# Optimization experiments

Measured on AMD Instinct MI355X. Metric: run time of the kernel, lower is better.

The kernel has to match this reference:

```python
import jax, jax.numpy as jnp
import numpy as np

B, H, E, D = 16384, 1024, 64, 128  # batch, hidden, nb_entities, wh_units==we_units


def setup_inputs() -> dict:
    key = jax.random.key(0)
    k0, k1, k2 = jax.random.split(key, 3)
    hidden_state = jax.random.normal(k0, (B, H), dtype=jnp.float32)
    # Wh: Dense(wh_units) acting on H -> D
    Wh_w = jax.random.normal(k1, (H, D), dtype=jnp.float32) * 0.02
    Wh_b = jnp.zeros((D,), dtype=jnp.float32)
    # We: nb_entities separate Dense(we_units), stacked into one [E, D, D] tensor
    We_w = jax.random.normal(k2, (E, D, D), dtype=jnp.float32) * 0.02
    We_b = jnp.zeros((E, D), dtype=jnp.float32)
    return {"hidden_state": hidden_state, "Wh_w": Wh_w, "Wh_b": Wh_b,
            "We_w": We_w, "We_b": We_b}


def reference(hidden_state, Wh_w, Wh_b, We_w, We_b):
    # reduced_dimentionality = Wh(hidden_state)            [B, D]
    r = hidden_state @ Wh_w + Wh_b
    # per-entity Dense loop + concat + transpose == one batched GEMM -> [B, E, D]
    logits = jnp.einsum('bk,ekd->bed', r, We_w) + We_b[None, :, :]
    outputs = jax.nn.softmax(logits, axis=-1)               # [B, E, D]
    # second pass: We[i] applied to outputs[:, i, :]       [B, E, D]
    vt = jnp.einsum('bek,ekd->bed', outputs, We_w) + We_b[None, :, :]
    # transpose to [B, D, E] then reduce_sum over E == sum over entity axis
    result = vt.sum(axis=1)                                 # [B, D]
    return (outputs, result)
```

## Files before the change

### kernel.cpp

```cpp
#include <hip/hip_runtime.h>
#include <hip/hip_bf16.h>

typedef __attribute__((ext_vector_type(8))) short short8;
typedef __attribute__((ext_vector_type(4))) float f32x4;
typedef __attribute__((ext_vector_type(4))) unsigned int uint4v;
typedef __attribute__((ext_vector_type(2))) unsigned int uint2v;

#define NB 16384
#define NH 1024
#define NE 64
#define ND 128
#define BR 32

static __device__ __forceinline__ unsigned short f2b(float x) {
  unsigned int u = __builtin_bit_cast(unsigned int, x);
  unsigned int r = (u + 0x7fffu + ((u >> 16) & 1u)) >> 16;
  return (unsigned short)r;
}
static __device__ __forceinline__ float b2f_lo(unsigned int u) {
  return __builtin_bit_cast(float, u << 16);
}
static __device__ __forceinline__ float b2f_hi(unsigned int u) {
  return __builtin_bit_cast(float, u & 0xffff0000u);
}

static __device__ __forceinline__ void bar_sync() {
  __builtin_amdgcn_sched_barrier(0);
  asm volatile("s_waitcnt lgkmcnt(0)" ::: "memory");
  __builtin_amdgcn_sched_barrier(0);
  __builtin_amdgcn_s_barrier();
  __builtin_amdgcn_sched_barrier(0);
}

static __device__ __forceinline__ int swz(int row, int col) {
  return (row << 7) + ((((col >> 3) ^ (row & 7)) << 3) | (col & 7));
}

__global__ __launch_bounds__(256, 1) void k0_prep(
    const float* __restrict__ Wh_w, const float* __restrict__ We_w,
    const float* __restrict__ We_b,
    unsigned short* __restrict__ WeT, unsigned short* __restrict__ WhT,
    float* __restrict__ bsum)
{
  __shared__ float tile[32][33];
  const int bid = blockIdx.x, t = threadIdx.x;
  const int i = t >> 5, j = t & 31;
  if (bid < 1024) {
    const int e = bid >> 4, tr = (bid >> 2) & 3, tc = bid & 3;
    const float* src = We_w + (size_t)e * 16384;
#pragma unroll
    for (int k = 0; k < 4; ++k)
      tile[i + 8 * k][j] = src[(size_t)(tr * 32 + i + 8 * k) * 128 + tc * 32 + j];
    __syncthreads();
    unsigned short* dst = WeT + (size_t)e * 16384;
#pragma unroll
    for (int k = 0; k < 4; ++k) {
      int row = i + 8 * k;
      dst[(size_t)(tc * 32 + row) * 128 + tr * 32 + j] = f2b(tile[j][row]);
    }
  } else if (bid < 1152) {
    const int tb = bid - 1024, tr = tb >> 2, tc = tb & 3;
#pragma unroll
    for (int k = 0; k < 4; ++k)
      tile[i + 8 * k][j] = Wh_w[(size_t)(tr * 32 + i + 8 * k) * 128 + tc * 32 + j];
    __syncthreads();
#pragma unroll
    for (int k = 0; k < 4; ++k) {
      int row = i + 8 * k;
      WhT[(size_t)(tc * 32 + row) * 1024 + tr * 32 + j] = f2b(tile[j][row]);
    }
  } else {
    if (t < 128) {
      float s = 0.f;
      for (int e = 0; e < 64; ++e) s += We_b[e * 128 + t];
      bsum[t] = s;
    }
  }
}

__global__ __launch_bounds__(256, 1) void k1_rgemm(
    const float* __restrict__ hidden, const unsigned short* __restrict__ WhT,
    const float* __restrict__ Wh_b, unsigned short* __restrict__ r_g)
{
  const int t = threadIdx.x;
  const int w = t >> 6, l = t & 63, c = l & 15, g = l >> 4;
  const int b = blockIdx.x * 64 + 16 * w + c;
  const float* hrow = hidden + (size_t)b * NH;
  f32x4 acc[8];
#pragma unroll
  for (int mf = 0; mf < 8; ++mf) acc[mf] = (f32x4){0.f, 0.f, 0.f, 0.f};
#pragma unroll 2
  for (int ks = 0; ks < 32; ++ks) {
    const int k0 = 8 * g + 32 * ks;
    f32x4 h0 = *(const f32x4*)(hrow + k0);
    f32x4 h1 = *(const f32x4*)(hrow + k0 + 4);
    short8 bf;
    bf[0] = (short)f2b(h0[0]); bf[1] = (short)f2b(h0[1]);
    bf[2] = (short)f2b(h0[2]); bf[3] = (short)f2b(h0[3]);
    bf[4] = (short)f2b(h1[0]); bf[5] = (short)f2b(h1[1]);
    bf[6] = (short)f2b(h1[2]); bf[7] = (short)f2b(h1[3]);
#pragma unroll
    for (int mf = 0; mf < 8; ++mf) {
      short8 af = *(const short8*)(WhT + (size_t)(c + 16 * mf) * NH + k0);
      acc[mf] = __builtin_amdgcn_mfma_f32_16x16x32_bf16(af, bf, acc[mf], 0, 0, 0);
    }
  }
#pragma unroll
  for (int mf = 0; mf < 8; ++mf) {
    const int d0 = 16 * mf + 4 * g;
    f32x4 bias = *(const f32x4*)(Wh_b + d0);
    f32x4 v = acc[mf] + bias;
    unsigned int lo = (unsigned)f2b(v[0]) | ((unsigned)f2b(v[1]) << 16);
    unsigned int hi = (unsigned)f2b(v[2]) | ((unsigned)f2b(v[3]) << 16);
    uint2v pk = {lo, hi};
    *(uint2v*)(r_g + (size_t)b * ND + d0) = pk;
  }
}

struct SmemK2 {
  union {
    struct {
      unsigned short r_lds[BR * 128];
      unsigned short P_lds[BR * 128];
    };
    float obuf[BR * 128];
  };
  float sms[4][BR];
};

static __device__ __forceinline__ void load_we_frags(
    short8 (&f)[2][4], f32x4 (&bias)[2],
    const unsigned short* __restrict__ WeT, const float* __restrict__ We_b,
    int e, int w, int c, int g)
{
  const unsigned short* base = WeT + (size_t)e * (ND * ND);
#pragma unroll
  for (int mf = 0; mf < 2; ++mf) {
    const unsigned short* rowp = base + (size_t)(16 * (2 * w + mf) + c) * ND + 8 * g;
#pragma unroll
    for (int ks = 0; ks < 4; ++ks)
      f[mf][ks] = *(const short8*)(rowp + 32 * ks);
    bias[mf] = *(const f32x4*)(We_b + e * ND + 32 * w + 16 * mf + 4 * g);
  }
}

static __device__ __forceinline__ void entity_body(
    int e, int en, int brow0, int w, int c, int g, int t,
    short8 (&cur)[2][4], short8 (&nxt)[2][4],
    f32x4 (&bcur)[2], f32x4 (&bnxt)[2], f32x4 (&acc2)[2][2],
    const unsigned short* __restrict__ WeT, const float* __restrict__ We_b,
    float* __restrict__ outP, SmemK2& sm)
{
  f32x4 acc1[2][2];
#pragma unroll
  for (int mf = 0; mf < 2; ++mf)
#pragma unroll
    for (int nf = 0; nf < 2; ++nf) acc1[mf][nf] = (f32x4){0.f, 0.f, 0.f, 0.f};
#pragma unroll
  for (int ks = 0; ks < 4; ++ks) {
    short8 b1[2];
#pragma unroll
    for (int nf = 0; nf < 2; ++nf)
      b1[nf] = *(const short8*)(&sm.r_lds[swz(16 * nf + c, 8 * g + 32 * ks)]);
#pragma unroll
    for (int mf = 0; mf < 2; ++mf)
#pragma unroll
      for (int nf = 0; nf < 2; ++nf)
        acc1[mf][nf] = __builtin_amdgcn_mfma_f32_16x16x32_bf16(
            cur[mf][ks], b1[nf], acc1[mf][nf], 0, 0, 0);
  }
  load_we_frags(nxt, bnxt, WeT, We_b, en, w, c, g);

#pragma unroll
  for (int mf = 0; mf < 2; ++mf)
#pragma unroll
    for (int nf = 0; nf < 2; ++nf) acc1[mf][nf] += bcur[mf];
  float s[2] = {0.f, 0.f};
#pragma unroll
  for (int nf = 0; nf < 2; ++nf) {
#pragma unroll
    for (int mf = 0; mf < 2; ++mf)
#pragma unroll
      for (int r = 0; r < 4; ++r) {
        float p = __expf(acc1[mf][nf][r]);
        acc1[mf][nf][r] = p;
        s[nf] += p;
      }
    s[nf] += __shfl_xor(s[nf], 16);
    s[nf] += __shfl_xor(s[nf], 32);
  }
  if (g == 0) {
#pragma unroll
    for (int nf = 0; nf < 2; ++nf) sm.sms[w][16 * nf + c] = s[nf];
  }
  bar_sync();
  float inv[2];
#pragma unroll
  for (int nf = 0; nf < 2; ++nf) {
    int b = 16 * nf + c;
    inv[nf] = 1.f / (sm.sms[0][b] + sm.sms[1][b] + sm.sms[2][b] + sm.sms[3][b]);
  }
#pragma unroll
  for (int mf = 0; mf < 2; ++mf)
#pragma unroll
    for (int nf = 0; nf < 2; ++nf) {
      f32x4 p = acc1[mf][nf] * inv[nf];
      unsigned int lo = (unsigned)f2b(p[0]) | ((unsigned)f2b(p[1]) << 16);
      unsigned int hi = (unsigned)f2b(p[2]) | ((unsigned)f2b(p[3]) << 16);
      uint2v pk = {lo, hi};
      *(uint2v*)(&sm.P_lds[swz(16 * nf + c, 32 * w + 16 * mf + 4 * g)]) = pk;
    }
  bar_sync();

  {
    const int orow = t >> 5;
    const int ocol = (t & 31) * 4;
#pragma unroll
    for (int it = 0; it < 4; ++it) {
      const int row = orow + 8 * it;
      uint2v u = *(const uint2v*)(&sm.P_lds[swz(row, ocol)]);
      f32x4 v;
      v[0] = b2f_lo(u[0]); v[1] = b2f_hi(u[0]);
      v[2] = b2f_lo(u[1]); v[3] = b2f_hi(u[1]);
      *(f32x4*)(outP + ((size_t)(brow0 + row) * NE + e) * ND + ocol) = v;
    }
  }
#pragma unroll
  for (int ks = 0; ks < 4; ++ks) {
    short8 a2[2];
#pragma unroll
    for (int mf2 = 0; mf2 < 2; ++mf2)
      a2[mf2] = *(const short8*)(&sm.P_lds[swz(16 * mf2 + c, 8 * g + 32 * ks)]);
#pragma unroll
    for (int mf2 = 0; mf2 < 2; ++mf2)
#pragma unroll
      for (int n = 0; n < 2; ++n)
        acc2[mf2][n] = __builtin_amdgcn_mfma_f32_16x16x32_bf16(
            a2[mf2], cur[n][ks], acc2[mf2][n], 0, 0, 0);
  }
}

__global__ __launch_bounds__(256, 3) void k2_main(
    const unsigned short* __restrict__ r_g, const unsigned short* __restrict__ WeT,
    const float* __restrict__ We_b, const float* __restrict__ bsum,
    float* __restrict__ outP, float* __restrict__ outR)
{
  __shared__ SmemK2 sm;
  const int t = threadIdx.x;
  const int w = t >> 6, l = t & 63, c = l & 15, g = l >> 4;
  const int brow0 = blockIdx.x * BR;
  const int e0 = (blockIdx.x & 3) << 4;

  for (int i = t; i < BR * 16; i += 256) {
    int row = i >> 4, ch = i & 15;
    uint4v v = *(const uint4v*)(r_g + (size_t)(brow0 + row) * ND + ch * 8);
    *(uint4v*)(&sm.r_lds[swz(row, ch * 8)]) = v;
  }
  const float bs0 = bsum[32 * w + c];
  const float bs1 = bsum[32 * w + 16 + c];

  f32x4 acc2[2][2];
#pragma unroll
  for (int i = 0; i < 2; ++i)
#pragma unroll
    for (int j = 0; j < 2; ++j) acc2[i][j] = (f32x4){0.f, 0.f, 0.f, 0.f};

  short8 wa[2][4], wb[2][4];
  f32x4 ba[2], bb[2];
  load_we_frags(wa, ba, WeT, We_b, e0, w, c, g);
  bar_sync();

  for (int i = 0; i < NE; i += 2) {
    const int eA = (e0 + i) & 63, eB = (e0 + i + 1) & 63, eC = (e0 + i + 2) & 63;
    entity_body(eA, eB, brow0, w, c, g, t, wa, wb, ba, bb, acc2, WeT, We_b, outP, sm);
    entity_body(eB, eC, brow0, w, c, g, t, wb, wa, bb, ba, acc2, WeT, We_b, outP, sm);
  }

  bar_sync();
#pragma unroll
  for (int mf2 = 0; mf2 < 2; ++mf2)
#pragma unroll
    for (int n = 0; n < 2; ++n) {
      float bs = n ? bs1 : bs0;
#pragma unroll
      for (int r = 0; r < 4; ++r)
        sm.obuf[(16 * mf2 + 4 * g + r) * ND + 32 * w + 16 * n + c] =
            acc2[mf2][n][r] + bs;
    }
  bar_sync();
  {
    const int orow = t >> 5, ocol = (t & 31) * 4;
#pragma unroll
    for (int it = 0; it < 4; ++it) {
      const int row = orow + 8 * it;
      *(f32x4*)(outR + (size_t)(brow0 + row) * ND + ocol) =
          *(const f32x4*)(&sm.obuf[row * ND + ocol]);
    }
  }
}

extern "C" void kernel_launch(void* const* d_in, const int* in_sizes, int n_in,
                              void* d_out, int out_size, void* d_ws, size_t ws_size,
                              hipStream_t stream)
{
  (void)in_sizes; (void)n_in; (void)out_size; (void)ws_size;
  const float* hidden = (const float*)d_in[0];
  const float* Wh_w   = (const float*)d_in[1];
  const float* Wh_b   = (const float*)d_in[2];
  const float* We_w   = (const float*)d_in[3];
  const float* We_b   = (const float*)d_in[4];
  float* outP = (float*)d_out;
  float* outR = outP + (size_t)NB * NE * ND;

  char* ws = (char*)d_ws;
  unsigned short* WeT = (unsigned short*)(ws);
  unsigned short* WhT = (unsigned short*)(ws + 2097152);
  unsigned short* r_g = (unsigned short*)(ws + 2097152 + 262144);
  float* bsum         = (float*)(ws + 2097152 + 262144 + 4194304);

  k0_prep<<<1153, 256, 0, stream>>>(Wh_w, We_w, We_b, WeT, WhT, bsum);
  k1_rgemm<<<256, 256, 0, stream>>>(hidden, WhT, Wh_b, r_g);
  k2_main<<<512, 256, 0, stream>>>(r_g, WeT, We_b, bsum, outP, outR);
}
```

Before: 278.6 us.

## Stage softmax outputs for 8 entities in LDS and write contiguous rows

Softmax probabilities for a group of 8 consecutive entities are now buffered in a larger LDS staging area, then written to global memory as contiguous 4 KB runs per batch row instead of 512 B per entity. This removes one barrier plus one scattered store phase per entity and makes the output writes more coalesced. Block-to-tile mapping is also remapped to spread entity start offsets and rows across the grid. The bigger LDS footprint lowers launch_bounds occupancy from 3 to 2 blocks per CU, and the swizzle now XORs with 16 rows instead of 8.

```diff
diff --git a/kernel.cpp b/kernel.cpp
--- a/kernel.cpp
+++ b/kernel.cpp
@@ -11,6 +11,7 @@
 #define NE 64
 #define ND 128
 #define BR 32
+#define GRP 8
 
 static __device__ __forceinline__ unsigned short f2b(float x) {
   unsigned int u = __builtin_bit_cast(unsigned int, x);
@@ -33,7 +34,10 @@
 }
 
 static __device__ __forceinline__ int swz(int row, int col) {
-  return (row << 7) + ((((col >> 3) ^ (row & 7)) << 3) | (col & 7));
+  return (row << 7) + ((((col >> 3) ^ (row & 15)) << 3) | (col & 7));
+}
+static __device__ __forceinline__ int pswz(int row, int eg, int col) {
+  return ((row * GRP + eg) << 7) + ((((col >> 3) ^ (row & 15)) << 3) | (col & 7));
 }
 
 __global__ __launch_bounds__(256, 1) void k0_prep(
@@ -119,12 +123,10 @@
 
 struct SmemK2 {
   union {
-    struct {
-      unsigned short r_lds[BR * 128];
-      unsigned short P_lds[BR * 128];
-    };
+    unsigned short Pst[BR * GRP * 128];
     float obuf[BR * 128];
   };
+  unsigned short r_lds[BR * 128];
   float sms[4][BR];
 };
 
@@ -145,11 +147,11 @@
 }
 
 static __device__ __forceinline__ void entity_body(
-    int e, int en, int brow0, int w, int c, int g, int t,
+    int eg, int en, int w, int c, int g,
     short8 (&cur)[2][4], short8 (&nxt)[2][4],
     f32x4 (&bcur)[2], f32x4 (&bnxt)[2], f32x4 (&acc2)[2][2],
     const unsigned short* __restrict__ WeT, const float* __restrict__ We_b,
-    float* __restrict__ outP, SmemK2& sm)
+    SmemK2& sm)
 {
   f32x4 acc1[2][2];
 #pragma unroll
@@ -208,29 +210,16 @@
       unsigned int lo = (unsigned)f2b(p[0]) | ((unsigned)f2b(p[1]) << 16);
       unsigned int hi = (unsigned)f2b(p[2]) | ((unsigned)f2b(p[3]) << 16);
       uint2v pk = {lo, hi};
-      *(uint2v*)(&sm.P_lds[swz(16 * nf + c, 32 * w + 16 * mf + 4 * g)]) = pk;
-    }
-  bar_sync();
-
-  {
-    const int orow = t >> 5;
-    const int ocol = (t & 31) * 4;
-#pragma unroll
-    for (int it = 0; it < 4; ++it) {
-      const int row = orow + 8 * it;
-      uint2v u = *(const uint2v*)(&sm.P_lds[swz(row, ocol)]);
-      f32x4 v;
-      v[0] = b2f_lo(u[0]); v[1] = b2f_hi(u[0]);
-      v[2] = b2f_lo(u[1]); v[3] = b2f_hi(u[1]);
-      *(f32x4*)(outP + ((size_t)(brow0 + row) * NE + e) * ND + ocol) = v;
-    }
-  }
+      *(uint2v*)(&sm.Pst[pswz(16 * nf + c, eg, 32 * w + 16 * mf + 4 * g)]) = pk;
+    }
+  bar_sync();
+
 #pragma unroll
   for (int ks = 0; ks < 4; ++ks) {
     short8 a2[2];
 #pragma unroll
     for (int mf2 = 0; mf2 < 2; ++mf2)
-      a2[mf2] = *(const short8*)(&sm.P_lds[swz(16 * mf2 + c, 8 * g + 32 * ks)]);
+      a2[mf2] = *(const short8*)(&sm.Pst[pswz(16 * mf2 + c, eg, 8 * g + 32 * ks)]);
 #pragma unroll
     for (int mf2 = 0; mf2 < 2; ++mf2)
 #pragma unroll
@@ -240,7 +229,7 @@
   }
 }
 
-__global__ __launch_bounds__(256, 3) void k2_main(
+__global__ __launch_bounds__(256, 2) void k2_main(
     const unsigned short* __restrict__ r_g, const unsigned short* __restrict__ WeT,
     const float* __restrict__ We_b, const float* __restrict__ bsum,
     float* __restrict__ outP, float* __restrict__ outR)
@@ -248,8 +237,9 @@
   __shared__ SmemK2 sm;
   const int t = threadIdx.x;
   const int w = t >> 6, l = t & 63, c = l & 15, g = l >> 4;
-  const int brow0 = blockIdx.x * BR;
-  const int e0 = (blockIdx.x & 3) << 4;
+  const int lb = (blockIdx.x & 7) * 64 + (blockIdx.x >> 3);
+  const int brow0 = lb * BR;
+  const int e0 = (((lb >> 6) + lb) & 7) << 3;
 
   for (int i = t; i < BR * 16; i += 256) {
     int row = i >> 4, ch = i & 15;
@@ -270,10 +260,32 @@
   load_we_frags(wa, ba, WeT, We_b, e0, w, c, g);
   bar_sync();
 
-  for (int i = 0; i < NE; i += 2) {
-    const int eA = (e0 + i) & 63, eB = (e0 + i + 1) & 63, eC = (e0 + i + 2) & 63;
-    entity_body(eA, eB, brow0, w, c, g, t, wa, wb, ba, bb, acc2, WeT, We_b, outP, sm);
-    entity_body(eB, eC, brow0, w, c, g, t, wb, wa, bb, ba, acc2, WeT, We_b, outP, sm);
+#pragma unroll 1
+  for (int gi = 0; gi < NE / GRP; ++gi) {
+    for (int j = 0; j < GRP; j += 2) {
+      const int i = gi * GRP + j;
+      const int eB = (e0 + i + 1) & 63, eC = (e0 + i + 2) & 63;
+      entity_body(j,     eB, w, c, g, wa, wb, ba, bb, acc2, WeT, We_b, sm);
+      entity_body(j + 1, eC, w, c, g, wb, wa, bb, ba, acc2, WeT, We_b, sm);
+    }
+    {
+      const int eg0 = (e0 + gi * GRP) & 63;
+#pragma unroll
+      for (int rr = 0; rr < 8; ++rr) {
+        const int row = 8 * w + rr;
+        float* dst = outP + ((size_t)(brow0 + row) * NE + eg0) * ND;
+#pragma unroll
+        for (int it = 0; it < 4; ++it) {
+          const int flat = it * 256 + l * 4;
+          const int eg = flat >> 7, col = flat & 127;
+          uint2v u = *(const uint2v*)(&sm.Pst[pswz(row, eg, col)]);
+          f32x4 v;
+          v[0] = b2f_lo(u[0]); v[1] = b2f_hi(u[0]);
+          v[2] = b2f_lo(u[1]); v[3] = b2f_hi(u[1]);
+          *(f32x4*)(dst + flat) = v;
+        }
+      }
+    }
   }
 
   bar_sync();
```

New measurement: 284.6 us. 2.2% more time.
